# Kernel optimization log

Hardware: AMD Instinct MI355X
Metric: run time of the kernel (lower is better)

Reference implementation:

```python
import jax, jax.numpy as jnp
import numpy as np

B = 256        # graph pairs
MAX_SET = 64   # nodes per graph == max_set_size (padding is identity)
E = 512        # edges per graph
D = 128        # node_state_dim == av.filters_3
T = 64         # av.transform_dim
N_PROP = 5
N_TIME = 3
TEMP = 0.1
SINK_ITERS = 20
NG = 2 * B
N = NG * MAX_SET
TOT_E = NG * E


def sinkhorn(log_alpha):
    la = log_alpha / TEMP
    for _ in range(SINK_ITERS):
        la = la - jax.nn.logsumexp(la, axis=2, keepdims=True)
        la = la - jax.nn.logsumexp(la, axis=1, keepdims=True)
    return jnp.exp(la)


def setup_inputs() -> dict:
    key = jax.random.key(0)
    ks = jax.random.split(key, 32)

    def lin(k, i, o):
        return jax.random.normal(k, (i, o), jnp.float32) / np.sqrt(i).astype(np.float32)

    node_features = jax.random.normal(ks[0], (N, 32), jnp.float32)
    edge_features = jax.random.normal(ks[1], (TOT_E, 16), jnp.float32)
    offs = jnp.repeat(jnp.arange(NG, dtype=jnp.int32) * MAX_SET, E)
    from_idx = jax.random.randint(ks[2], (TOT_E,), 0, MAX_SET, jnp.int32) + offs
    to_idx = jax.random.randint(ks[3], (TOT_E,), 0, MAX_SET, jnp.int32) + offs
    return {
        "node_features": node_features, "edge_features": edge_features,
        "from_idx": from_idx, "to_idx": to_idx,
        "node_enc_w": lin(ks[4], 32, D), "node_enc_b": jnp.zeros((D,), jnp.float32),
        "edge_enc_w": lin(ks[5], 16, 64), "edge_enc_b": jnp.zeros((64,), jnp.float32),
        "mw1": lin(ks[6], 2 * D + 64, 2 * D), "mb1": jnp.zeros((2 * D,), jnp.float32),
        "mw2": lin(ks[7], 2 * D, D), "mb2": jnp.zeros((D,), jnp.float32),
        "nw1": lin(ks[8], 2 * D, 2 * D), "nb1": jnp.zeros((2 * D,), jnp.float32),
        "nw2": lin(ks[9], 2 * D, D), "nb2": jnp.zeros((D,), jnp.float32),
        "cw1": lin(ks[10], 2 * D, 2 * D), "cb1": jnp.zeros((2 * D,), jnp.float32),
        "cw2": lin(ks[11], 2 * D, D), "cb2": jnp.zeros((D,), jnp.float32),
        "t1w": lin(ks[12], D, T), "t1b": jnp.zeros((T,), jnp.float32),
        "t2w": lin(ks[13], T, T), "t2b": jnp.zeros((T,), jnp.float32),
    }


def reference(node_features, edge_features, from_idx, to_idx,
              node_enc_w, node_enc_b, edge_enc_w, edge_enc_b,
              mw1, mb1, mw2, mb2, nw1, nb1, nw2, nb2,
              cw1, cb1, cw2, cb2, t1w, t1b, t2w, t2b):
    # Encoder (GMN GraphEncoder: linear maps on raw node/edge features)
    h0 = node_features @ node_enc_w + node_enc_b          # [N, D]
    e0 = edge_features @ edge_enc_w + edge_enc_b          # [TOT_E, 64]
    store = jnp.zeros((N, D * (N_PROP + 1)), h0.dtype)    # node_feature_store
    plan = None
    for _t in range(N_TIME):
        h = h0
        parts = [jnp.zeros((N, D), h0.dtype)]             # slot 0 stays zero
        for p in range(1, N_PROP + 1):
            inter = store[:, (p - 1) * D: p * D]          # time_update_idx == 'k_t'
            comb = jax.nn.relu(jnp.concatenate([h, inter], 1) @ cw1 + cb1) @ cw2 + cb2
            # GraphPropLayer: gather -> message MLP -> segment_sum -> node update MLP
            msg_in = jnp.concatenate([comb[from_idx], comb[to_idx], e0], 1)
            messages = jax.nn.relu(msg_in @ mw1 + mb1) @ mw2 + mb2
            agg = jax.ops.segment_sum(messages, to_idx, num_segments=N)
            h = jax.nn.relu(jnp.concatenate([comb, agg], 1) @ nw1 + nb1) @ nw2 + nb2
            parts.append(h)
        store = jnp.concatenate(parts, 1)                 # [N, D*(K+1)]
        # split into padded query/corpus stacks (all graphs have MAX_SET nodes,
        # so F.pad and the size masks are identity here)
        s = store.reshape(NG, MAX_SET, -1)
        q, c = s[0::2], s[1::2]                           # [B, M, D*(K+1)]
        tq = jax.nn.relu(q[:, :, -D:] @ t1w + t1b) @ t2w + t2b
        tc = jax.nn.relu(c[:, :, -D:] @ t1w + t1b) @ t2w + t2b
        sim = jnp.einsum('bqt,bct->bqc', tq, tc)
        plan = sinkhorn(sim)                              # node transport plan [B,M,M]
        qfc = jnp.einsum('bqc,bcd->bqd', plan, c)
        cfq = jnp.einsum('bqc,bqd->bcd', plan, q)
        inter_feats = jnp.stack([qfc, cfq], 1)[:, :, :, D:].reshape(N, N_PROP * D)
        store = store.at[:, D:].set(inter_feats)
    return plan
```

## Files before the change

### kernel.cpp

```cpp
#include <hip/hip_runtime.h>
#include <hip/hip_bf16.h>

#define NNODES   32768
#define NGROUPS  512
#define EPG      512
#define ND       (32768l*128)

typedef __attribute__((ext_vector_type(4))) float f32x4;
typedef __attribute__((ext_vector_type(8))) short bf16x8;

__device__ __forceinline__ short f2bf(float x) {
  unsigned u = __float_as_uint(x);
  unsigned r = (u + 0x7FFF + ((u >> 16) & 1)) >> 16;
  return (short)r;
}
__device__ __forceinline__ float bf2f(short h) {
  return __uint_as_float(((unsigned)(unsigned short)h) << 16);
}
__device__ __forceinline__ void split3(float x, short* ph, short* pm, short* pl, long idx) {
  short h = f2bf(x); float r1 = x - bf2f(h);
  short m = f2bf(r1); float r2 = r1 - bf2f(m);
  ph[idx] = h; pm[idx] = m; pl[idx] = f2bf(r2);
}

__global__ void k_node_enc(const float* __restrict__ nf, const float* __restrict__ w,
                           const float* __restrict__ b, float* __restrict__ h0) {
  int idx = blockIdx.x * 256 + threadIdx.x;
  int row = idx >> 7, col = idx & 127;
  const float* x = nf + row * 32;
  float acc = b[col];
#pragma unroll
  for (int k = 0; k < 32; ++k) acc = fmaf(x[k], w[k * 128 + col], acc);
  h0[idx] = acc;
}

__global__ void k_prep(const float* __restrict__ eew, const float* __restrict__ eeb,
                       const float* __restrict__ mw1, const float* __restrict__ mb1,
                       const float* __restrict__ mb2, const float* __restrict__ nw1,
                       float* __restrict__ Wfold, float* __restrict__ bfold,
                       float* __restrict__ vbias) {
  const int c = threadIdx.x, b = blockIdx.x;
  if (b < 16) {
    float a = 0.f;
    for (int j = 0; j < 64; ++j) a = fmaf(eew[b * 64 + j], mw1[(256 + j) * 256 + c], a);
    Wfold[b * 256 + c] = a;
  } else if (b == 16) {
    float a = mb1[c];
    for (int j = 0; j < 64; ++j) a = fmaf(eeb[j], mw1[(256 + j) * 256 + c], a);
    bfold[c] = a;
  } else {
    float a = 0.f;
    for (int j = 0; j < 128; ++j) a = fmaf(mb2[j], nw1[(128 + j) * 256 + c], a);
    vbias[c] = a;
  }
}

__global__ void k_wsplit3(const float* __restrict__ W, int C, int Kd,
                          short* __restrict__ th, short* __restrict__ tm,
                          short* __restrict__ tl) {
  const int c = blockIdx.x;
  for (int k = threadIdx.x; k < Kd; k += 256) {
    float w = W[(long)k * C + c];
    split3(w, th, tm, tl, c * 256 + k);
  }
}

__global__ void k_csr(const int* __restrict__ from_idx, const int* __restrict__ to_idx,
                      const float* __restrict__ ef,
                      int* __restrict__ csr_f, int* __restrict__ rp_g,
                      float* __restrict__ efp, int* __restrict__ deg) {
  __shared__ int cnt[64], rps[65];
  __shared__ int tls[EPG], fls[EPG];
  __shared__ short ord[EPG];
  const int g = blockIdx.x, tid = threadIdx.x;
  const int be = g * EPG, bn = g * 64;
  if (tid < 64) cnt[tid] = 0;
  __syncthreads();
  for (int e = tid; e < EPG; e += 256) {
    int t = to_idx[be + e] - bn;
    tls[e] = t;
    fls[e] = from_idx[be + e] - bn;
    atomicAdd(&cnt[t], 1);
  }
  __syncthreads();
  if (tid == 0) {
    int s = 0;
    for (int i = 0; i < 64; ++i) { rps[i] = s; s += cnt[i]; }
    rps[64] = s;
  }
  __syncthreads();
  if (tid < 64) {
    int pos = rps[tid];
    for (int e = 0; e < EPG; ++e)
      if (tls[e] == tid) ord[pos++] = (short)e;
  }
  __syncthreads();
  for (int ec = tid; ec < EPG; ec += 256) {
    const int eo = ord[ec];
    csr_f[be + ec] = fls[eo];
    const float4* src = (const float4*)&ef[(long)(be + eo) * 16];
    float4* dst = (float4*)&efp[(long)(be + ec) * 16];
    dst[0] = src[0]; dst[1] = src[1]; dst[2] = src[2]; dst[3] = src[3];
  }
  if (tid < 65) rp_g[g * 65 + tid] = rps[tid];
  if (tid < 64) deg[bn + tid] = cnt[tid];
}

template<int KTOT, bool DEG, bool SUM2, bool RPX0, bool WPOUT>
__global__ __launch_bounds__(256, 3)
void k_mlp2m(const float* __restrict__ x0,
             const short* __restrict__ x0h, const short* __restrict__ x0m,
             const short* __restrict__ x0l,
             const float* __restrict__ x1, const float* __restrict__ x1b,
             const short* __restrict__ W1h, const short* __restrict__ W1m,
             const short* __restrict__ W1l,
             const float* __restrict__ b1, const int* __restrict__ deg,
             const float* __restrict__ vbias,
             const short* __restrict__ W2h, const short* __restrict__ W2m,
             const short* __restrict__ W2l,
             const float* __restrict__ b2,
             float* __restrict__ out,
             short* __restrict__ outh, short* __restrict__ outm,
             short* __restrict__ outl) {
  __shared__ short xh[32 * 264];
  __shared__ short xm[32 * 264];
  __shared__ short xl[32 * 264];
  __shared__ int degs[32];
  const int tid = threadIdx.x;
  const long row0 = (long)blockIdx.x * 32;

  if constexpr (RPX0) {
    for (int i = tid; i < 32 * 16; i += 256) {
      const int r = i >> 4, q = i & 15;
      const long gb = (row0 + r) * 128 + q * 8;
      const int lb = r * 264 + q * 8;
      *(bf16x8*)&xh[lb] = *(const bf16x8*)&x0h[gb];
      *(bf16x8*)&xm[lb] = *(const bf16x8*)&x0m[gb];
      *(bf16x8*)&xl[lb] = *(const bf16x8*)&x0l[gb];
    }
  } else {
    for (int i = tid; i < 32 * 32; i += 256) {
      const int r = i >> 5, q = i & 31;
      float4 v = *(const float4*)&x0[(row0 + r) * 128 + q * 4];
      const int base = r * 264 + q * 4;
      split3(v.x, xh, xm, xl, base + 0);
      split3(v.y, xh, xm, xl, base + 1);
      split3(v.z, xh, xm, xl, base + 2);
      split3(v.w, xh, xm, xl, base + 3);
    }
  }
  if constexpr (KTOT == 256) {
    for (int i = tid; i < 32 * 32; i += 256) {
      const int r = i >> 5, q = i & 31;
      float4 v = *(const float4*)&x1[(row0 + r) * 128 + q * 4];
      if constexpr (SUM2) {
        float4 w = *(const float4*)&x1b[(row0 + r) * 128 + q * 4];
        v.x += w.x; v.y += w.y; v.z += w.z; v.w += w.w;
      }
      const int base = r * 264 + 128 + q * 4;
      split3(v.x, xh, xm, xl, base + 0);
      split3(v.y, xh, xm, xl, base + 1);
      split3(v.z, xh, xm, xl, base + 2);
      split3(v.w, xh, xm, xl, base + 3);
    }
  }
  if constexpr (DEG) { if (tid < 32) degs[tid] = deg[row0 + tid]; }
  __syncthreads();

  const int lane = tid & 63, wid = tid >> 6;
  const int lr = lane & 15;
  const int lk = (lane >> 4) * 8;
  const int rsub = (lane >> 4) * 4;

  f32x4 acc[2][4];
#pragma unroll
  for (int fc = 0; fc < 4; ++fc) {
    const int col = wid * 64 + fc * 16 + lr;
    const float bv = b1[col];
#pragma unroll
    for (int fr = 0; fr < 2; ++fr) acc[fr][fc] = {bv, bv, bv, bv};
    if constexpr (DEG) {
      const float vb = vbias[col];
#pragma unroll
      for (int fr = 0; fr < 2; ++fr)
#pragma unroll
        for (int r = 0; r < 4; ++r)
          acc[fr][fc][r] += (float)degs[fr * 16 + rsub + r] * vb;
    }
  }

#pragma unroll 2
  for (int ks = 0; ks < KTOT / 32; ++ks) {
    const int k0 = ks * 32 + lk;
    bf16x8 ah[2], am[2], al[2];
#pragma unroll
    for (int fr = 0; fr < 2; ++fr) {
      const int ab = (fr * 16 + lr) * 264 + k0;
      ah[fr] = *(const bf16x8*)&xh[ab];
      am[fr] = *(const bf16x8*)&xm[ab];
      al[fr] = *(const bf16x8*)&xl[ab];
    }
#pragma unroll
    for (int fc = 0; fc < 4; ++fc) {
      const long wrow = (long)(wid * 64 + fc * 16 + lr) * 256 + k0;
      const bf16x8 bh = *(const bf16x8*)&W1h[wrow];
      const bf16x8 bm = *(const bf16x8*)&W1m[wrow];
      const bf16x8 bl = *(const bf16x8*)&W1l[wrow];
#pragma unroll
      for (int fr = 0; fr < 2; ++fr) {
        acc[fr][fc] = __builtin_amdgcn_mfma_f32_16x16x32_bf16(ah[fr], bh, acc[fr][fc], 0, 0, 0);
        acc[fr][fc] = __builtin_amdgcn_mfma_f32_16x16x32_bf16(ah[fr], bm, acc[fr][fc], 0, 0, 0);
        acc[fr][fc] = __builtin_amdgcn_mfma_f32_16x16x32_bf16(am[fr], bh, acc[fr][fc], 0, 0, 0);
        acc[fr][fc] = __builtin_amdgcn_mfma_f32_16x16x32_bf16(ah[fr], bl, acc[fr][fc], 0, 0, 0);
        acc[fr][fc] = __builtin_amdgcn_mfma_f32_16x16x32_bf16(am[fr], bm, acc[fr][fc], 0, 0, 0);
        acc[fr][fc] = __builtin_amdgcn_mfma_f32_16x16x32_bf16(al[fr], bh, acc[fr][fc], 0, 0, 0);
      }
    }
  }
  __syncthreads();

#pragma unroll
  for (int fr = 0; fr < 2; ++fr)
#pragma unroll
    for (int fc = 0; fc < 4; ++fc) {
      const int col = wid * 64 + fc * 16 + lr;
#pragma unroll
      for (int r = 0; r < 4; ++r) {
        const int row = fr * 16 + rsub + r;
        float v = fmaxf(acc[fr][fc][r], 0.f);
        split3(v, xh, xm, xl, row * 264 + col);
      }
    }
  __syncthreads();

  f32x4 acc2[2][2];
#pragma unroll
  for (int fc = 0; fc < 2; ++fc) {
    const float bv = b2[wid * 32 + fc * 16 + lr];
#pragma unroll
    for (int fr = 0; fr < 2; ++fr) acc2[fr][fc] = {bv, bv, bv, bv};
  }
#pragma unroll 2
  for (int ks = 0; ks < 8; ++ks) {
    const int k0 = ks * 32 + lk;
    bf16x8 ah[2], am[2], al[2];
#pragma unroll
    for (int fr = 0; fr < 2; ++fr) {
      const int ab = (fr * 16 + lr) * 264 + k0;
      ah[fr] = *(const bf16x8*)&xh[ab];
      am[fr] = *(const bf16x8*)&xm[ab];
      al[fr] = *(const bf16x8*)&xl[ab];
    }
#pragma unroll
    for (int fc = 0; fc < 2; ++fc) {
      const long wrow = (long)(wid * 32 + fc * 16 + lr) * 256 + k0;
      const bf16x8 bh = *(const bf16x8*)&W2h[wrow];
      const bf16x8 bm = *(const bf16x8*)&W2m[wrow];
      const bf16x8 bl = *(const bf16x8*)&W2l[wrow];
#pragma unroll
      for (int fr = 0; fr < 2; ++fr) {
        acc2[fr][fc] = __builtin_amdgcn_mfma_f32_16x16x32_bf16(ah[fr], bh, acc2[fr][fc], 0, 0, 0);
        acc2[fr][fc] = __builtin_amdgcn_mfma_f32_16x16x32_bf16(ah[fr], bm, acc2[fr][fc], 0, 0, 0);
        acc2[fr][fc] = __builtin_amdgcn_mfma_f32_16x16x32_bf16(am[fr], bh, acc2[fr][fc], 0, 0, 0);
        acc2[fr][fc] = __builtin_amdgcn_mfma_f32_16x16x32_bf16(ah[fr], bl, acc2[fr][fc], 0, 0, 0);
        acc2[fr][fc] = __builtin_amdgcn_mfma_f32_16x16x32_bf16(am[fr], bm, acc2[fr][fc], 0, 0, 0);
        acc2[fr][fc] = __builtin_amdgcn_mfma_f32_16x16x32_bf16(al[fr], bh, acc2[fr][fc], 0, 0, 0);
      }
    }
  }
#pragma unroll
  for (int fr = 0; fr < 2; ++fr)
#pragma unroll
    for (int fc = 0; fc < 2; ++fc) {
      const int col = wid * 32 + fc * 16 + lr;
#pragma unroll
      for (int r = 0; r < 4; ++r) {
        const long gi = (row0 + fr * 16 + rsub + r) * 128 + col;
        if constexpr (WPOUT) {
          split3(acc2[fr][fc][r], outh, outm, outl, gi);
        } else {
          out[gi] = acc2[fr][fc][r];
        }
      }
    }
}

__global__ __attribute__((amdgpu_waves_per_eu(2, 2))) __launch_bounds__(256)
void k_edgem(const short* __restrict__ chp, const short* __restrict__ cmp,
             const short* __restrict__ clp,
             const float* __restrict__ efp,
             const short* __restrict__ m1h, const short* __restrict__ m1m,
             const short* __restrict__ m1l,
             const short* __restrict__ m2h, const short* __restrict__ m2m,
             const short* __restrict__ m2l,
             const float* __restrict__ Wfold, const float* __restrict__ bfold,
             const int* __restrict__ csr_f, const int* __restrict__ rp_g,
             float* __restrict__ aggM) {
  __shared__ __align__(16) float cAB[2 * 64 * 68];
  __shared__ __align__(16) float ag2[2][64 * 68];
  __shared__ int fl[EPG];
  __shared__ int rp[65];
  float* cA = cAB;
  float* cB = cAB + 64 * 68;
  short* agp = (short*)cAB;

  const int tid = threadIdx.x;
  const int g = blockIdx.x, half = blockIdx.y;
  const int be = g * EPG, bn = g * 64;

  for (int i = tid; i < EPG; i += 256) fl[i] = csr_f[be + i];
  if (tid < 65) rp[tid] = rp_g[g * 65 + tid];

  const int lane = tid & 63, wid = tid >> 6;
  const int lr = lane & 15;
  const int lk = (lane >> 4) * 8;
  const int rsub = (lane >> 4) * 4;
  const int ng = tid >> 4, cg = tid & 15;
  const int n0 = ng * 4, cq = cg * 4;

  for (int cbi = 0; cbi < 2; ++cbi) {
    const int col0 = (half * 2 + cbi) * 64;
    __syncthreads();

    {
      const int isB = wid >> 1;
      const int cw = (wid & 1) * 32;
      const int wkof = isB * 128;
      float* dstC = isB ? cB : cA;
#pragma unroll 1
      for (int hf = 0; hf < 2; ++hf) {
        f32x4 c[2][2];
#pragma unroll
        for (int fr = 0; fr < 2; ++fr)
#pragma unroll
          for (int fc = 0; fc < 2; ++fc) c[fr][fc] = {0.f, 0.f, 0.f, 0.f};
        for (int ks = 0; ks < 4; ++ks) {
          const int k0 = ks * 32 + lk;
          bf16x8 ah[2], am[2], al[2];
#pragma unroll
          for (int fr = 0; fr < 2; ++fr) {
            const long ga = (long)(bn + (hf * 2 + fr) * 16 + lr) * 128 + k0;
            ah[fr] = *(const bf16x8*)&chp[ga];
            am[fr] = *(const bf16x8*)&cmp[ga];
            al[fr] = *(const bf16x8*)&clp[ga];
          }
#pragma unroll
          for (int fc = 0; fc < 2; ++fc) {
            const long wrow = (long)(col0 + cw + fc * 16 + lr) * 256 + wkof + k0;
            const bf16x8 bh = *(const bf16x8*)&m1h[wrow];
            const bf16x8 bm = *(const bf16x8*)&m1m[wrow];
            const bf16x8 bl = *(const bf16x8*)&m1l[wrow];
#pragma unroll
            for (int fr = 0; fr < 2; ++fr) {
              c[fr][fc] = __builtin_amdgcn_mfma_f32_16x16x32_bf16(ah[fr], bh, c[fr][fc], 0, 0, 0);
              c[fr][fc] = __builtin_amdgcn_mfma_f32_16x16x32_bf16(ah[fr], bm, c[fr][fc], 0, 0, 0);
              c[fr][fc] = __builtin_amdgcn_mfma_f32_16x16x32_bf16(am[fr], bh, c[fr][fc], 0, 0, 0);
              c[fr][fc] = __builtin_amdgcn_mfma_f32_16x16x32_bf16(ah[fr], bl, c[fr][fc], 0, 0, 0);
              c[fr][fc] = __builtin_amdgcn_mfma_f32_16x16x32_bf16(am[fr], bm, c[fr][fc], 0, 0, 0);
              c[fr][fc] = __builtin_amdgcn_mfma_f32_16x16x32_bf16(al[fr], bh, c[fr][fc], 0, 0, 0);
            }
          }
        }
#pragma unroll
        for (int fr = 0; fr < 2; ++fr)
#pragma unroll
          for (int fc = 0; fc < 2; ++fc) {
            const int col = cw + fc * 16 + lr;
#pragma unroll
            for (int r = 0; r < 4; ++r)
              dstC[((hf * 2 + fr) * 16 + rsub + r) * 68 + col] = c[fr][fc][r];
          }
      }
    }
    float4 Wf[16];
#pragma unroll
    for (int k = 0; k < 16; ++k) Wf[k] = *(const float4*)&Wfold[k * 256 + col0 + cq];
    const float4 bf = *(const float4*)&bfold[col0 + cq];
    __syncthreads();

#pragma unroll
    for (int i = 0; i < 4; ++i) {
      const int n = n0 + i;
      const float4 cBn = *(const float4*)&cB[n * 68 + cq];
      const int eBeg = rp[n], eEnd = rp[n + 1];
      float4 acc0 = make_float4(0.f, 0.f, 0.f, 0.f);
      float4 acc1 = make_float4(0.f, 0.f, 0.f, 0.f);
      int e = eBeg;
      for (; e + 1 < eEnd; e += 2) {
        const int f0 = fl[e], f1 = fl[e + 1];
        const float* er0 = efp + (long)(be + e) * 16;
        const float* er1 = efp + (long)(be + e + 1) * 16;
        float4 ea[4], eb[4];
#pragma unroll
        for (int kq = 0; kq < 4; ++kq) { ea[kq] = ((const float4*)er0)[kq]; eb[kq] = ((const float4*)er1)[kq]; }
        float4 h0 = bf, h1 = bf;
#pragma unroll
        for (int kq = 0; kq < 4; ++kq) {
          const float ev0[4] = {ea[kq].x, ea[kq].y, ea[kq].z, ea[kq].w};
          const float ev1[4] = {eb[kq].x, eb[kq].y, eb[kq].z, eb[kq].w};
#pragma unroll
          for (int s = 0; s < 4; ++s) {
            const float4 w = Wf[kq * 4 + s];
            h0.x = fmaf(ev0[s], w.x, h0.x); h0.y = fmaf(ev0[s], w.y, h0.y);
            h0.z = fmaf(ev0[s], w.z, h0.z); h0.w = fmaf(ev0[s], w.w, h0.w);
            h1.x = fmaf(ev1[s], w.x, h1.x); h1.y = fmaf(ev1[s], w.y, h1.y);
            h1.z = fmaf(ev1[s], w.z, h1.z); h1.w = fmaf(ev1[s], w.w, h1.w);
          }
        }
        const float4 va0 = *(const float4*)&cA[f0 * 68 + cq];
        const float4 va1 = *(const float4*)&cA[f1 * 68 + cq];
        acc0.x += fmaxf(h0.x + va0.x + cBn.x, 0.f);
        acc0.y += fmaxf(h0.y + va0.y + cBn.y, 0.f);
        acc0.z += fmaxf(h0.z + va0.z + cBn.z, 0.f);
        acc0.w += fmaxf(h0.w + va0.w + cBn.w, 0.f);
        acc1.x += fmaxf(h1.x + va1.x + cBn.x, 0.f);
        acc1.y += fmaxf(h1.y + va1.y + cBn.y, 0.f);
        acc1.z += fmaxf(h1.z + va1.z + cBn.z, 0.f);
        acc1.w += fmaxf(h1.w + va1.w + cBn.w, 0.f);
      }
      if (e < eEnd) {
        const int f = fl[e];
        const float* er = efp + (long)(be + e) * 16;
        float4 h = bf;
#pragma unroll
        for (int kq = 0; kq < 4; ++kq) {
          const float4 e4 = ((const float4*)er)[kq];
          const float ev[4] = {e4.x, e4.y, e4.z, e4.w};
#pragma unroll
          for (int s = 0; s < 4; ++s) {
            const float4 w = Wf[kq * 4 + s];
            h.x = fmaf(ev[s], w.x, h.x); h.y = fmaf(ev[s], w.y, h.y);
            h.z = fmaf(ev[s], w.z, h.z); h.w = fmaf(ev[s], w.w, h.w);
          }
        }
        const float4 va = *(const float4*)&cA[f * 68 + cq];
        acc0.x += fmaxf(h.x + va.x + cBn.x, 0.f);
        acc0.y += fmaxf(h.y + va.y + cBn.y, 0.f);
        acc0.z += fmaxf(h.z + va.z + cBn.z, 0.f);
        acc0.w += fmaxf(h.w + va.w + cBn.w, 0.f);
      }
      acc0.x += acc1.x; acc0.y += acc1.y; acc0.z += acc1.z; acc0.w += acc1.w;
      *(float4*)&ag2[cbi][n * 68 + cq] = acc0;
    }
  }
  __syncthreads();

  f32x4 aM[4][2];
#pragma unroll
  for (int fr = 0; fr < 4; ++fr)
#pragma unroll
    for (int fc = 0; fc < 2; ++fc) aM[fr][fc] = {0.f, 0.f, 0.f, 0.f};

  for (int cbi = 0; cbi < 2; ++cbi) {
    const int col0 = (half * 2 + cbi) * 64;
    for (int i = tid; i < 1024; i += 256) {
      const int n = i >> 4, kq = (i & 15) * 4;
      const float4 v = *(const float4*)&ag2[cbi][n * 68 + kq];
      const int b0 = n * 72 + kq;
      split3(v.x, agp, agp + 4608, agp + 9216, b0 + 0);
      split3(v.y, agp, agp + 4608, agp + 9216, b0 + 1);
      split3(v.z, agp, agp + 4608, agp + 9216, b0 + 2);
      split3(v.w, agp, agp + 4608, agp + 9216, b0 + 3);
    }
    __syncthreads();

    for (int ks = 0; ks < 2; ++ks) {
      const int k0 = ks * 32 + lk;
      bf16x8 ah[4], am[4], al[4];
#pragma unroll
      for (int fr = 0; fr < 4; ++fr) {
        const int ab = (fr * 16 + lr) * 72 + k0;
        ah[fr] = *(const bf16x8*)&agp[ab];
        am[fr] = *(const bf16x8*)&agp[4608 + ab];
        al[fr] = *(const bf16x8*)&agp[9216 + ab];
      }
#pragma unroll
      for (int fc = 0; fc < 2; ++fc) {
        const long wrow = (long)(wid * 32 + fc * 16 + lr) * 256 + col0 + k0;
        const bf16x8 bh = *(const bf16x8*)&m2h[wrow];
        const bf16x8 bm = *(const bf16x8*)&m2m[wrow];
        const bf16x8 bl = *(const bf16x8*)&m2l[wrow];
#pragma unroll
        for (int fr = 0; fr < 4; ++fr) {
          aM[fr][fc] = __builtin_amdgcn_mfma_f32_16x16x32_bf16(ah[fr], bh, aM[fr][fc], 0, 0, 0);
          aM[fr][fc] = __builtin_amdgcn_mfma_f32_16x16x32_bf16(ah[fr], bm, aM[fr][fc], 0, 0, 0);
          aM[fr][fc] = __builtin_amdgcn_mfma_f32_16x16x32_bf16(am[fr], bh, aM[fr][fc], 0, 0, 0);
          aM[fr][fc] = __builtin_amdgcn_mfma_f32_16x16x32_bf16(ah[fr], bl, aM[fr][fc], 0, 0, 0);
          aM[fr][fc] = __builtin_amdgcn_mfma_f32_16x16x32_bf16(am[fr], bm, aM[fr][fc], 0, 0, 0);
          aM[fr][fc] = __builtin_amdgcn_mfma_f32_16x16x32_bf16(al[fr], bh, aM[fr][fc], 0, 0, 0);
        }
      }
    }
    __syncthreads();
  }

  float* aggMh = aggM + (long)half * ND;
#pragma unroll
  for (int fr = 0; fr < 4; ++fr)
#pragma unroll
    for (int fc = 0; fc < 2; ++fc) {
      const int col = wid * 32 + fc * 16 + lr;
#pragma unroll
      for (int r = 0; r < 4; ++r)
        aggMh[(long)(bn + fr * 16 + rsub + r) * 128 + col] = aM[fr][fc][r];
    }
}

__global__ void k_tfeat(const float* __restrict__ x,
                        const float* __restrict__ t1w, const float* __restrict__ t1b,
                        const float* __restrict__ t2w, const float* __restrict__ t2b,
                        float* __restrict__ tf) {
  __shared__ float xs[4][128];
  __shared__ float ys[4][64];
  const int tid = threadIdx.x;
  const long row0 = (long)blockIdx.x * 4;
  for (int i = tid; i < 512; i += 256)
    xs[i >> 7][i & 127] = x[(row0 + (i >> 7)) * 128 + (i & 127)];
  __syncthreads();
  const int r = tid >> 6, c = tid & 63;
  float acc = t1b[c];
#pragma unroll 4
  for (int k = 0; k < 128; ++k) acc = fmaf(xs[r][k], t1w[k * 64 + c], acc);
  ys[r][c] = fmaxf(acc, 0.f);
  __syncthreads();
  float a2 = t2b[c];
#pragma unroll 4
  for (int k = 0; k < 64; ++k) a2 = fmaf(ys[r][k], t2w[k * 64 + c], a2);
  tf[(row0 + r) * 64 + c] = a2;
}

__global__ void k_sim(const float* __restrict__ tf, float* __restrict__ sim) {
  const int b = blockIdx.x, tid = threadIdx.x;
  __shared__ float tq[64][65];
  __shared__ float tcs[64][65];
  for (int i = tid; i < 4096; i += 256) {
    tq[i >> 6][i & 63]  = tf[(long)b * 8192 + i];
    tcs[i >> 6][i & 63] = tf[(long)b * 8192 + 4096 + i];
  }
  __syncthreads();
  const int m = tid >> 2, j0 = (tid & 3) * 16;
#pragma unroll
  for (int j = 0; j < 16; ++j) {
    float a = 0.f;
#pragma unroll 4
    for (int k = 0; k < 64; ++k) a = fmaf(tq[m][k], tcs[j0 + j][k], a);
    sim[(long)b * 4096 + m * 64 + j0 + j] = a;
  }
}

__global__ void k_sink(float* __restrict__ sim, float* __restrict__ outp) {
  const int b = blockIdx.x, tid = threadIdx.x;
  __shared__ float la[64][65];
  const float C = 14.426950408889634f;
  for (int i = tid; i < 4096; i += 256)
    la[i >> 6][i & 63] = sim[(long)b * 4096 + i] * C;
  __syncthreads();
  const int r4 = tid >> 2, l4 = tid & 3;
  for (int it = 0; it < 20; ++it) {
    {
      float m = -3.4e38f;
#pragma unroll
      for (int i = 0; i < 16; ++i) m = fmaxf(m, la[r4][l4 + 4 * i]);
      m = fmaxf(m, __shfl_xor(m, 1)); m = fmaxf(m, __shfl_xor(m, 2));
      float s = 0.f;
#pragma unroll
      for (int i = 0; i < 16; ++i) s += exp2f(la[r4][l4 + 4 * i] - m);
      s += __shfl_xor(s, 1); s += __shfl_xor(s, 2);
      const float lse = m + log2f(s);
#pragma unroll
      for (int i = 0; i < 16; ++i) la[r4][l4 + 4 * i] -= lse;
    }
    __syncthreads();
    {
      float m = -3.4e38f;
#pragma unroll
      for (int i = 0; i < 16; ++i) m = fmaxf(m, la[l4 + 4 * i][r4]);
      m = fmaxf(m, __shfl_xor(m, 1)); m = fmaxf(m, __shfl_xor(m, 2));
      float s = 0.f;
#pragma unroll
      for (int i = 0; i < 16; ++i) s += exp2f(la[l4 + 4 * i][r4] - m);
      s += __shfl_xor(s, 1); s += __shfl_xor(s, 2);
      const float lse = m + log2f(s);
#pragma unroll
      for (int i = 0; i < 16; ++i) la[l4 + 4 * i][r4] -= lse;
    }
    __syncthreads();
  }
  for (int i = tid; i < 4096; i += 256) {
    const float v = exp2f(la[i >> 6][i & 63]);
    outp[(long)b * 4096 + i] = v;
    sim[(long)b * 4096 + i] = v;
  }
}

__global__ void k_mix(const float* __restrict__ plan, const float* __restrict__ src,
                      float* __restrict__ dst) {
  const int b = blockIdx.x, tid = threadIdx.x;
  __shared__ float pl[64][65];
  __shared__ float qs[64][128];
  __shared__ float cs[64][128];
  const long qbase = (long)(2 * b) * 64, cbase = qbase + 64;
  for (int i = tid; i < 4096; i += 256) pl[i >> 6][i & 63] = plan[(long)b * 4096 + i];
  for (int i = tid; i < 8192; i += 256) {
    qs[i >> 7][i & 127] = src[qbase * 128 + i];
    cs[i >> 7][i & 127] = src[cbase * 128 + i];
  }
  __syncthreads();
  const int d = tid & 127, m0 = (tid >> 7) * 32;
  for (int m = m0; m < m0 + 32; ++m) {
    float a = 0.f;
#pragma unroll 4
    for (int j = 0; j < 64; ++j) a = fmaf(pl[m][j], cs[j][d], a);
    dst[(qbase + m) * 128 + d] = a;
  }
  for (int j = m0; j < m0 + 32; ++j) {
    float a = 0.f;
#pragma unroll 4
    for (int m = 0; m < 64; ++m) a = fmaf(pl[m][j], qs[m][d], a);
    dst[(cbase + j) * 128 + d] = a;
  }
}

extern "C" void kernel_launch(void* const* d_in, const int* in_sizes, int n_in,
                              void* d_out, int out_size, void* d_ws, size_t ws_size,
                              hipStream_t stream) {
  const float* nf  = (const float*)d_in[0];
  const float* ef  = (const float*)d_in[1];
  const int* from_idx = (const int*)d_in[2];
  const int* to_idx   = (const int*)d_in[3];
  const float* new_w = (const float*)d_in[4];
  const float* new_b = (const float*)d_in[5];
  const float* eew = (const float*)d_in[6];
  const float* eeb = (const float*)d_in[7];
  const float* mw1 = (const float*)d_in[8];
  const float* mb1 = (const float*)d_in[9];
  const float* mw2 = (const float*)d_in[10];
  const float* mb2 = (const float*)d_in[11];
  const float* nw1 = (const float*)d_in[12];
  const float* nb1 = (const float*)d_in[13];
  const float* nw2 = (const float*)d_in[14];
  const float* nb2 = (const float*)d_in[15];
  const float* cw1 = (const float*)d_in[16];
  const float* cb1 = (const float*)d_in[17];
  const float* cw2 = (const float*)d_in[18];
  const float* cb2 = (const float*)d_in[19];
  const float* t1w = (const float*)d_in[20];
  const float* t1b = (const float*)d_in[21];
  const float* t2w = (const float*)d_in[22];
  const float* t2b = (const float*)d_in[23];

  float* W = (float*)d_ws;
  float* h0     = W;
  float* aggM0  = h0 + ND;
  float* aggM1  = aggM0 + ND;
  float* parts  = aggM1 + ND;
  float* efp    = parts + 5 * ND;
  float* Wfold  = efp + 262144l * 16;
  float* bfold  = Wfold + 4096;
  float* vbias  = bfold + 256;
  int*   deg    = (int*)(vbias + 256);
  int*   csr_f  = deg + 32768;
  int*   rp_g   = csr_f + 262144;
  short* cw1t_h = (short*)(rp_g + 33280);
  short* cw1t_m = cw1t_h + 65536;
  short* cw1t_l = cw1t_m + 65536;
  short* nw1t_h = cw1t_l + 65536;
  short* nw1t_m = nw1t_h + 65536;
  short* nw1t_l = nw1t_m + 65536;
  short* cw2t_h = nw1t_l + 65536;
  short* cw2t_m = cw2t_h + 32768;
  short* cw2t_l = cw2t_m + 32768;
  short* nw2t_h = cw2t_l + 32768;
  short* nw2t_m = nw2t_h + 32768;
  short* nw2t_l = nw2t_m + 32768;
  short* m1t_h  = nw2t_l + 32768;
  short* m1t_m  = m1t_h + 65536;
  short* m1t_l  = m1t_m + 65536;
  short* m2t_h  = m1t_l + 65536;
  short* m2t_m  = m2t_h + 32768;
  short* m2t_l  = m2t_m + 32768;
  short* chp    = m2t_l + 32768;
  short* cmp    = chp + 32768l * 128;
  short* clp    = cmp + 32768l * 128;
  float* tf     = aggM0;
  float* sim    = aggM0 + 2097152;
  float* outp   = (float*)d_out;

  k_prep<<<18, 256, 0, stream>>>(eew, eeb, mw1, mb1, mb2, nw1, Wfold, bfold, vbias);
  k_csr<<<512, 256, 0, stream>>>(from_idx, to_idx, ef, csr_f, rp_g, efp, deg);
  k_wsplit3<<<256, 256, 0, stream>>>(cw1, 256, 256, cw1t_h, cw1t_m, cw1t_l);
  k_wsplit3<<<256, 256, 0, stream>>>(nw1, 256, 256, nw1t_h, nw1t_m, nw1t_l);
  k_wsplit3<<<128, 256, 0, stream>>>(cw2, 128, 256, cw2t_h, cw2t_m, cw2t_l);
  k_wsplit3<<<128, 256, 0, stream>>>(nw2, 128, 256, nw2t_h, nw2t_m, nw2t_l);
  k_wsplit3<<<256, 256, 0, stream>>>(mw1, 256, 256, m1t_h, m1t_m, m1t_l);
  k_wsplit3<<<128, 256, 0, stream>>>(mw2, 128, 256, m2t_h, m2t_m, m2t_l);
  k_node_enc<<<16384, 256, 0, stream>>>(nf, new_w, new_b, h0);

  for (int t = 0; t < 3; ++t) {
    const float* hprev = h0;
    for (int p = 1; p <= 5; ++p) {
      if (t > 0 && p > 1)
        k_mlp2m<256, false, false, false, true><<<1024, 256, 0, stream>>>(
            hprev, nullptr, nullptr, nullptr,
            parts + (long)(p - 1) * ND, nullptr,
            cw1t_h, cw1t_m, cw1t_l, cb1, nullptr, nullptr,
            cw2t_h, cw2t_m, cw2t_l, cb2, nullptr, chp, cmp, clp);
      else
        k_mlp2m<128, false, false, false, true><<<1024, 256, 0, stream>>>(
            hprev, nullptr, nullptr, nullptr, nullptr, nullptr,
            cw1t_h, cw1t_m, cw1t_l, cb1, nullptr, nullptr,
            cw2t_h, cw2t_m, cw2t_l, cb2, nullptr, chp, cmp, clp);
      k_edgem<<<dim3(512, 2), 256, 0, stream>>>(chp, cmp, clp, efp,
                                                m1t_h, m1t_m, m1t_l,
                                                m2t_h, m2t_m, m2t_l,
                                                Wfold, bfold, csr_f, rp_g, aggM0);
      float* hnew = parts + (long)(p - 1) * ND;
      k_mlp2m<256, true, true, true, false><<<1024, 256, 0, stream>>>(
          nullptr, chp, cmp, clp, aggM0, aggM1,
          nw1t_h, nw1t_m, nw1t_l, nb1, deg, vbias,
          nw2t_h, nw2t_m, nw2t_l, nb2, hnew, nullptr, nullptr, nullptr);
      hprev = hnew;
    }
    k_tfeat<<<8192, 256, 0, stream>>>(parts + 4 * ND, t1w, t1b, t2w, t2b, tf);
    k_sim<<<256, 256, 0, stream>>>(tf, sim);
    k_sink<<<256, 256, 0, stream>>>(sim, outp);
    if (t < 2) {
      for (int pi = 3; pi >= 0; --pi)
        k_mix<<<256, 256, 0, stream>>>(sim, parts + (long)pi * ND, parts + (long)(pi + 1) * ND);
    }
  }
}
```

Baseline: 5.599 ms.

## Interleave per-chunk mw2 MFMA with aggregation to cut LDS and raise occupancy

The second-layer message MFMA now runs inside each 64-column chunk loop instead of after both chunks, so only one aggregation buffer is kept in shared memory. The from-index list is stored as shorts. The launch bound changes from two waves per EU to a minimum of three blocks per CU. The first chunk writes its partial result to global memory and the second adds to it with global atomics. This trades some extra global traffic and atomic cost for less LDS use and higher occupancy.

```diff
diff --git a/kernel.cpp b/kernel.cpp
--- a/kernel.cpp
+++ b/kernel.cpp
@@ -285,7 +285,7 @@
     }
 }
 
-__global__ __attribute__((amdgpu_waves_per_eu(2, 2))) __launch_bounds__(256)
+__global__ __launch_bounds__(256, 3)
 void k_edgem(const short* __restrict__ chp, const short* __restrict__ cmp,
              const short* __restrict__ clp,
              const float* __restrict__ efp,
@@ -297,8 +297,8 @@
              const int* __restrict__ csr_f, const int* __restrict__ rp_g,
              float* __restrict__ aggM) {
   __shared__ __align__(16) float cAB[2 * 64 * 68];
-  __shared__ __align__(16) float ag2[2][64 * 68];
-  __shared__ int fl[EPG];
+  __shared__ __align__(16) float ag[64 * 64];
+  __shared__ short fl[EPG];
   __shared__ int rp[65];
   float* cA = cAB;
   float* cB = cAB + 64 * 68;
@@ -308,7 +308,7 @@
   const int g = blockIdx.x, half = blockIdx.y;
   const int be = g * EPG, bn = g * 64;
 
-  for (int i = tid; i < EPG; i += 256) fl[i] = csr_f[be + i];
+  for (int i = tid; i < EPG; i += 256) fl[i] = (short)csr_f[be + i];
   if (tid < 65) rp[tid] = rp_g[g * 65 + tid];
 
   const int lane = tid & 63, wid = tid >> 6;
@@ -317,6 +317,8 @@
   const int rsub = (lane >> 4) * 4;
   const int ng = tid >> 4, cg = tid & 15;
   const int n0 = ng * 4, cq = cg * 4;
+
+  float* aggMh = aggM + (long)half * ND;
 
   for (int cbi = 0; cbi < 2; ++cbi) {
     const int col0 = (half * 2 + cbi) * 64;
@@ -440,22 +442,13 @@
         acc0.w += fmaxf(h.w + va.w + cBn.w, 0.f);
       }
       acc0.x += acc1.x; acc0.y += acc1.y; acc0.z += acc1.z; acc0.w += acc1.w;
-      *(float4*)&ag2[cbi][n * 68 + cq] = acc0;
-    }
-  }
-  __syncthreads();
-
-  f32x4 aM[4][2];
-#pragma unroll
-  for (int fr = 0; fr < 4; ++fr)
-#pragma unroll
-    for (int fc = 0; fc < 2; ++fc) aM[fr][fc] = {0.f, 0.f, 0.f, 0.f};
-
-  for (int cbi = 0; cbi < 2; ++cbi) {
-    const int col0 = (half * 2 + cbi) * 64;
+      *(float4*)&ag[n * 64 + cq] = acc0;
+    }
+    __syncthreads();
+
     for (int i = tid; i < 1024; i += 256) {
       const int n = i >> 4, kq = (i & 15) * 4;
-      const float4 v = *(const float4*)&ag2[cbi][n * 68 + kq];
+      const float4 v = *(const float4*)&ag[n * 64 + kq];
       const int b0 = n * 72 + kq;
       split3(v.x, agp, agp + 4608, agp + 9216, b0 + 0);
       split3(v.y, agp, agp + 4608, agp + 9216, b0 + 1);
@@ -464,46 +457,63 @@
     }
     __syncthreads();
 
-    for (int ks = 0; ks < 2; ++ks) {
-      const int k0 = ks * 32 + lk;
-      bf16x8 ah[4], am[4], al[4];
-#pragma unroll
-      for (int fr = 0; fr < 4; ++fr) {
-        const int ab = (fr * 16 + lr) * 72 + k0;
-        ah[fr] = *(const bf16x8*)&agp[ab];
-        am[fr] = *(const bf16x8*)&agp[4608 + ab];
-        al[fr] = *(const bf16x8*)&agp[9216 + ab];
-      }
-#pragma unroll
-      for (int fc = 0; fc < 2; ++fc) {
-        const long wrow = (long)(wid * 32 + fc * 16 + lr) * 256 + col0 + k0;
-        const bf16x8 bh = *(const bf16x8*)&m2h[wrow];
-        const bf16x8 bm = *(const bf16x8*)&m2m[wrow];
-        const bf16x8 bl = *(const bf16x8*)&m2l[wrow];
+    {
+      f32x4 aM2[4][2];
+#pragma unroll
+      for (int fr = 0; fr < 4; ++fr)
+#pragma unroll
+        for (int fc = 0; fc < 2; ++fc) aM2[fr][fc] = {0.f, 0.f, 0.f, 0.f};
+
+      for (int ks = 0; ks < 2; ++ks) {
+        const int k0 = ks * 32 + lk;
+        bf16x8 ah[4], am[4], al[4];
 #pragma unroll
         for (int fr = 0; fr < 4; ++fr) {
-          aM[fr][fc] = __builtin_amdgcn_mfma_f32_16x16x32_bf16(ah[fr], bh, aM[fr][fc], 0, 0, 0);
-          aM[fr][fc] = __builtin_amdgcn_mfma_f32_16x16x32_bf16(ah[fr], bm, aM[fr][fc], 0, 0, 0);
-          aM[fr][fc] = __builtin_amdgcn_mfma_f32_16x16x32_bf16(am[fr], bh, aM[fr][fc], 0, 0, 0);
-          aM[fr][fc] = __builtin_amdgcn_mfma_f32_16x16x32_bf16(ah[fr], bl, aM[fr][fc], 0, 0, 0);
-          aM[fr][fc] = __builtin_amdgcn_mfma_f32_16x16x32_bf16(am[fr], bm, aM[fr][fc], 0, 0, 0);
-          aM[fr][fc] = __builtin_amdgcn_mfma_f32_16x16x32_bf16(al[fr], bh, aM[fr][fc], 0, 0, 0);
+          const int ab = (fr * 16 + lr) * 72 + k0;
+          ah[fr] = *(const bf16x8*)&agp[ab];
+          am[fr] = *(const bf16x8*)&agp[4608 + ab];
+          al[fr] = *(const bf16x8*)&agp[9216 + ab];
         }
-      }
-    }
-    __syncthreads();
-  }
-
-  float* aggMh = aggM + (long)half * ND;
-#pragma unroll
-  for (int fr = 0; fr < 4; ++fr)
-#pragma unroll
-    for (int fc = 0; fc < 2; ++fc) {
-      const int col = wid * 32 + fc * 16 + lr;
-#pragma unroll
-      for (int r = 0; r < 4; ++r)
-        aggMh[(long)(bn + fr * 16 + rsub + r) * 128 + col] = aM[fr][fc][r];
-    }
+#pragma unroll
+        for (int fc = 0; fc < 2; ++fc) {
+          const long wrow = (long)(wid * 32 + fc * 16 + lr) * 256 + col0 + k0;
+          const bf16x8 bh = *(const bf16x8*)&m2h[wrow];
+          const bf16x8 bm = *(const bf16x8*)&m2m[wrow];
+          const bf16x8 bl = *(const bf16x8*)&m2l[wrow];
+#pragma unroll
+          for (int fr = 0; fr < 4; ++fr) {
+            aM2[fr][fc] = __builtin_amdgcn_mfma_f32_16x16x32_bf16(ah[fr], bh, aM2[fr][fc], 0, 0, 0);
+            aM2[fr][fc] = __builtin_amdgcn_mfma_f32_16x16x32_bf16(ah[fr], bm, aM2[fr][fc], 0, 0, 0);
+            aM2[fr][fc] = __builtin_amdgcn_mfma_f32_16x16x32_bf16(am[fr], bh, aM2[fr][fc], 0, 0, 0);
+            aM2[fr][fc] = __builtin_amdgcn_mfma_f32_16x16x32_bf16(ah[fr], bl, aM2[fr][fc], 0, 0, 0);
+            aM2[fr][fc] = __builtin_amdgcn_mfma_f32_16x16x32_bf16(am[fr], bm, aM2[fr][fc], 0, 0, 0);
+            aM2[fr][fc] = __builtin_amdgcn_mfma_f32_16x16x32_bf16(al[fr], bh, aM2[fr][fc], 0, 0, 0);
+          }
+        }
+      }
+      if (cbi == 0) {
+#pragma unroll
+        for (int fr = 0; fr < 4; ++fr)
+#pragma unroll
+          for (int fc = 0; fc < 2; ++fc) {
+            const int col = wid * 32 + fc * 16 + lr;
+#pragma unroll
+            for (int r = 0; r < 4; ++r)
+              aggMh[(long)(bn + fr * 16 + rsub + r) * 128 + col] = aM2[fr][fc][r];
+          }
+      } else {
+#pragma unroll
+        for (int fr = 0; fr < 4; ++fr)
+#pragma unroll
+          for (int fc = 0; fc < 2; ++fc) {
+            const int col = wid * 32 + fc * 16 + lr;
+#pragma unroll
+            for (int r = 0; r < 4; ++r)
+              atomicAdd(&aggMh[(long)(bn + fr * 16 + rsub + r) * 128 + col], aM2[fr][fc][r]);
+          }
+      }
+    }
+  }
 }
 
 __global__ void k_tfeat(const float* __restrict__ x,
```

After: 6.118 ms. 9.3% more time.
